# Optimization experiments

Measured on AMD Instinct MI355X. Metric: run time of the kernel, lower is better.

The kernel has to match this reference:

```python
import jax, jax.numpy as jnp
import numpy as np

DIM = 512
HEADS = 8
DIM_HEAD = 64
INNER = HEADS * DIM_HEAD  # 512
EPS = 1e-5


def _per_head_layernorm(t, gamma, beta):
    # t: [b, h, n, k]; gamma/beta: [h, k] (distinct LayerNorm per head)
    mu = jnp.mean(t, axis=-1, keepdims=True)
    var = jnp.mean(jnp.square(t - mu), axis=-1, keepdims=True)
    t_hat = (t - mu) * jax.lax.rsqrt(var + EPS)
    return t_hat * gamma[None, :, None, :] + beta[None, :, None, :]


def setup_inputs() -> dict:
    key = jax.random.key(0)
    ks = jax.random.split(key, 6)
    x = jax.random.normal(ks[0], (4, 8192, DIM), dtype=jnp.float32)
    # xavier_normal_ with gain=1e-4 on to_qkv weight [3*inner, dim]
    std_qkv = 1e-4 * np.sqrt(2.0 / (3 * INNER + DIM))
    W_qkv = jax.random.normal(ks[1], (3 * INNER, DIM), dtype=jnp.float32) * std_qkv
    gamma_K = jnp.ones((HEADS, DIM_HEAD), dtype=jnp.float32)
    beta_K = jnp.zeros((HEADS, DIM_HEAD), dtype=jnp.float32)
    gamma_V = jnp.ones((HEADS, DIM_HEAD), dtype=jnp.float32)
    beta_V = jnp.zeros((HEADS, DIM_HEAD), dtype=jnp.float32)
    std_out = np.sqrt(1.0 / INNER)
    W_out = jax.random.uniform(ks[2], (DIM, INNER), dtype=jnp.float32, minval=-std_out, maxval=std_out)
    b_out = jax.random.uniform(ks[3], (DIM,), dtype=jnp.float32, minval=-std_out, maxval=std_out)
    return {"x": x, "W_qkv": W_qkv, "gamma_K": gamma_K, "beta_K": beta_K,
            "gamma_V": gamma_V, "beta_V": beta_V, "W_out": W_out, "b_out": b_out}


def reference(x, W_qkv, gamma_K, beta_K, gamma_V, beta_V, W_out, b_out):
    b, n, _ = x.shape
    qkv = jnp.einsum('bnd,ed->bne', x, W_qkv)  # [b, n, 3*inner]
    q, k, v = jnp.split(qkv, 3, axis=-1)

    def to_heads(t):  # [b, n, h*k] -> [b, h, n, k]
        return t.reshape(b, n, HEADS, DIM_HEAD).transpose(0, 2, 1, 3)

    q, k, v = to_heads(q), to_heads(k), to_heads(v)
    k = _per_head_layernorm(k, gamma_K, beta_K)
    v = _per_head_layernorm(v, gamma_V, beta_V)

    # Galerkin linear attention: (K^T V)/n then Q @ (.)  -> O(n * d^2)
    p_attn = jnp.einsum('bhnk,bhnv->bhkv', k, v) / n  # [b, h, k, k]
    out = jnp.einsum('bhnk,bhkv->bhnv', q, p_attn)    # [b, h, n, k]
    out = out.transpose(0, 2, 1, 3).reshape(b, n, INNER)
    return jnp.einsum('bne,de->bnd', out, W_out) + b_out
```

## Files before the change

kernel.cpp:

```cpp
#include <hip/hip_runtime.h>


typedef __attribute__((ext_vector_type(8))) short bf16x8;
typedef __attribute__((ext_vector_type(4))) float f32x4;
typedef __attribute__((ext_vector_type(4))) unsigned short u16x4;

__device__ __forceinline__ unsigned short f2bf(float f) {
  unsigned int u = __builtin_bit_cast(unsigned int, f);
  u += 0x7FFFu + ((u >> 16) & 1u);
  return (unsigned short)(u >> 16);
}

__device__ __forceinline__ f32x4 mfma16(bf16x8 a, bf16x8 b, f32x4 c) {
  return __builtin_amdgcn_mfma_f32_16x16x32_bf16(a, b, c, 0, 0, 0);
}

__device__ __forceinline__ void gload16(const void* g, void* l) {
  __builtin_amdgcn_global_load_lds(
      (const __attribute__((address_space(1))) void*)g,
      (__attribute__((address_space(3))) void*)l, 16, 0, 0);
}

__global__ void k_cvt_bf16(const float* __restrict__ src,
                           unsigned short* __restrict__ dst, int n4) {
  int i = blockIdx.x * blockDim.x + threadIdx.x;
  if (i < n4) {
    float4 v = ((const float4*)src)[i];
    u16x4 o;
    o[0] = f2bf(v.x); o[1] = f2bf(v.y); o[2] = f2bf(v.z); o[3] = f2bf(v.w);
    ((u16x4*)dst)[i] = o;
  }
}

__device__ __forceinline__ void stage_tile(const unsigned short* pa,
                                           const unsigned short* pb,
                                           unsigned short* As, unsigned short* Bs,
                                           int w) {
#pragma unroll
  for (int j = 0; j < 4; ++j) {
    gload16(pa + j * 8 * 512, As + w * 2048 + j * 512);
    gload16(pb + j * 8 * 512, Bs + w * 2048 + j * 512);
  }
}

__device__ __forceinline__ void compute_tile(const unsigned short* As,
                                             const unsigned short* Bs,
                                             int wr, int wc, int g, int c16,
                                             f32x4 acc[4][4]) {
#pragma unroll
  for (int ks = 0; ks < 2; ++ks) {
    const int kcol = (ks * 32 + g * 8) ^ ((c16 & 7) << 3);
    bf16x8 af[4], bfv[4];
#pragma unroll
    for (int mi = 0; mi < 4; ++mi)
      af[mi] = *(const bf16x8*)&As[(wr * 64 + mi * 16 + c16) * 64 + kcol];
#pragma unroll
    for (int ni = 0; ni < 4; ++ni)
      bfv[ni] = *(const bf16x8*)&Bs[(wc * 64 + ni * 16 + c16) * 64 + kcol];
#pragma unroll
    for (int mi = 0; mi < 4; ++mi)
#pragma unroll
      for (int ni = 0; ni < 4; ++ni)
        acc[mi][ni] = mfma16(af[mi], bfv[ni], acc[mi][ni]);
  }
}

__launch_bounds__(256)
__global__ void k1_kvp(const unsigned short* __restrict__ xb,
                       const unsigned short* __restrict__ wqkvb,
                       const float* __restrict__ gK, const float* __restrict__ bK,
                       const float* __restrict__ gV, const float* __restrict__ bV,
                       float* __restrict__ P) {
  __shared__ __align__(16) unsigned short As[2][8192];
  __shared__ __align__(16) unsigned short Bs[2][8192];
  const int rt = blockIdx.x, h = blockIdx.y;
  const int tid = (int)threadIdx.x;
  const int l = tid & 63, w = tid >> 6;
  const int wr = w >> 1, wc = w & 1;
  const int g = l >> 4, c16 = l & 15;
  const int row0 = rt * 128;
  const int swz = ((l & 7) ^ (l >> 3)) * 8;

  const unsigned short* gsA = xb + (row0 + w * 32 + (l >> 3)) * 512 + swz;
  const int bcol = (w < 2) ? (512 + h * 64 + w * 32) : (1024 + h * 64 + (w - 2) * 32);
  const unsigned short* gsB = wqkvb + (bcol + (l >> 3)) * 512 + swz;

  f32x4 acc[4][4] = {};
  stage_tile(gsA, gsB, As[0], Bs[0], w);
  __syncthreads();
  for (int kt = 0; kt < 7; ++kt) {
    stage_tile(gsA + (kt + 1) * 64, gsB + (kt + 1) * 64,
               As[(kt + 1) & 1], Bs[(kt + 1) & 1], w);
    compute_tile(As[kt & 1], Bs[kt & 1], wr, wc, g, c16, acc);
    __syncthreads();
  }
  compute_tile(As[1], Bs[1], wr, wc, g, c16, acc);

  const float* gamma = (wc == 0) ? gK : gV;
  const float* beta  = (wc == 0) ? bK : bV;
  float gm[4], bt[4];
#pragma unroll
  for (int ni = 0; ni < 4; ++ni) {
    gm[ni] = gamma[h * 64 + ni * 16 + c16];
    bt[ni] = beta[h * 64 + ni * 16 + c16];
  }

  unsigned short* Kl = &As[0][0];
  unsigned short* Vl = &Bs[0][0];
  unsigned short* dst = (wc == 0) ? Kl : Vl;

#pragma unroll
  for (int mi = 0; mi < 4; ++mi) {
    float mean4[4], rs4[4];
#pragma unroll
    for (int r = 0; r < 4; ++r) {
      float a0 = acc[mi][0][r], a1 = acc[mi][1][r];
      float a2 = acc[mi][2][r], a3 = acc[mi][3][r];
      float s1 = a0 + a1 + a2 + a3;
      float s2 = a0 * a0 + a1 * a1 + a2 * a2 + a3 * a3;
#pragma unroll
      for (int m = 1; m <= 8; m <<= 1) {
        s1 += __shfl_xor(s1, m, 64);
        s2 += __shfl_xor(s2, m, 64);
      }
      const float mean = s1 * (1.0f / 64.0f);
      const float var = s2 * (1.0f / 64.0f) - mean * mean;
      mean4[r] = mean;
      rs4[r] = rsqrtf(var + 1e-5f);
    }
    const int n0 = wr * 64 + mi * 16 + g * 4;
#pragma unroll
    for (int ni = 0; ni < 4; ++ni) {
      const int d = ni * 16 + c16;
      u16x4 o;
#pragma unroll
      for (int r = 0; r < 4; ++r)
        o[r] = f2bf((acc[mi][ni][r] - mean4[r]) * rs4[r] * gm[ni] + bt[ni]);
      *(u16x4*)&dst[d * 128 + (((n0 >> 3) ^ c16) << 3) + (n0 & 7)] = o;
    }
  }
  __syncthreads();

  f32x4 pacc[4] = {};
#pragma unroll
  for (int ks = 0; ks < 4; ++ks) {
    const int p8 = (ks * 4 + g);
    bf16x8 af = *(const bf16x8*)&Kl[(w * 16 + c16) * 128 + ((p8 ^ c16) << 3)];
#pragma unroll
    for (int ni = 0; ni < 4; ++ni) {
      bf16x8 bfv = *(const bf16x8*)&Vl[(ni * 16 + c16) * 128 + ((p8 ^ c16) << 3)];
      pacc[ni] = mfma16(af, bfv, pacc[ni]);
    }
  }
  const int bh = (row0 >> 13) * 8 + h;
  float* Pp = P + bh * 4096;
#pragma unroll
  for (int ni = 0; ni < 4; ++ni)
#pragma unroll
    for (int r = 0; r < 4; ++r)
      atomicAdd(&Pp[(w * 16 + g * 4 + r) * 64 + ni * 16 + c16], pacc[ni][r]);
}

__launch_bounds__(256)
__global__ void k3a_g(const float* __restrict__ Wqkv,
                      const float* __restrict__ P,
                      unsigned short* __restrict__ Gt) {
  __shared__ float Pl[64 * 64];
  const int bh = blockIdx.x, dd = blockIdx.y;
  const int b = bh >> 3, h = bh & 7;
  const int t = (int)threadIdx.x;
  for (int i = t; i < 1024; i += 256)
    ((float4*)Pl)[i] = ((const float4*)(P + bh * 4096))[i];
  __syncthreads();

  const int qg = t >> 6, dl = t & 63;
  const int d = dd * 64 + dl;
  float acc[16] = {};
  for (int dh = 0; dh < 64; ++dh) {
    const float wq = Wqkv[(h * 64 + dh) * 512 + d];
    const float* pr = &Pl[dh * 64 + qg * 16];
#pragma unroll
    for (int i = 0; i < 16; ++i) acc[i] += pr[i] * wq;
  }
  unsigned short* go = &Gt[(b * 512 + d) * 512 + h * 64 + qg * 16];
#pragma unroll
  for (int i = 0; i < 16; ++i) go[i] = f2bf(acc[i] * (1.0f / 8192.0f));
}

__launch_bounds__(256)
__global__ void k3b_m(const unsigned short* __restrict__ wob,
                      const unsigned short* __restrict__ Gt,
                      unsigned short* __restrict__ Mb) {
  __shared__ __align__(16) unsigned short As[2][8192];
  __shared__ __align__(16) unsigned short Bs[2][8192];
  const int rt = blockIdx.x, ct = blockIdx.y, b = blockIdx.z;
  const int tid = (int)threadIdx.x;
  const int l = tid & 63, w = tid >> 6;
  const int wr = w >> 1, wc = w & 1;
  const int g = l >> 4, c16 = l & 15;
  const int row0 = rt * 128, col0 = ct * 128;
  const int swz = ((l & 7) ^ (l >> 3)) * 8;

  const unsigned short* gsA = wob + (row0 + w * 32 + (l >> 3)) * 512 + swz;
  const unsigned short* gsB = Gt + b * 262144 + (col0 + w * 32 + (l >> 3)) * 512 + swz;

  f32x4 acc[4][4] = {};
  stage_tile(gsA, gsB, As[0], Bs[0], w);
  __syncthreads();
  for (int kt = 0; kt < 7; ++kt) {
    stage_tile(gsA + (kt + 1) * 64, gsB + (kt + 1) * 64,
               As[(kt + 1) & 1], Bs[(kt + 1) & 1], w);
    compute_tile(As[kt & 1], Bs[kt & 1], wr, wc, g, c16, acc);
    __syncthreads();
  }
  compute_tile(As[1], Bs[1], wr, wc, g, c16, acc);

#pragma unroll
  for (int mi = 0; mi < 4; ++mi)
#pragma unroll
    for (int ni = 0; ni < 4; ++ni) {
      const int colg = col0 + wc * 64 + ni * 16 + c16;
#pragma unroll
      for (int r = 0; r < 4; ++r) {
        const int rowg = row0 + wr * 64 + mi * 16 + g * 4 + r;
        Mb[(b * 512 + rowg) * 512 + colg] = f2bf(acc[mi][ni][r]);
      }
    }
}

__launch_bounds__(256)
__global__ void k4_final(const unsigned short* __restrict__ xb,
                         const unsigned short* __restrict__ Mb,
                         const float* __restrict__ bout,
                         float* __restrict__ y) {
  __shared__ __align__(16) unsigned short As[2][8192];
  __shared__ __align__(16) unsigned short Bs[2][8192];
  const int rt = blockIdx.x, ct = blockIdx.y;
  const int tid = (int)threadIdx.x;
  const int l = tid & 63, w = tid >> 6;
  const int wr = w >> 1, wc = w & 1;
  const int g = l >> 4, c16 = l & 15;
  const int row0 = rt * 128, col0 = ct * 128;
  const int bb = row0 >> 13;
  const int swz = ((l & 7) ^ (l >> 3)) * 8;

  const unsigned short* gsA = xb + (row0 + w * 32 + (l >> 3)) * 512 + swz;
  const unsigned short* gsB = Mb + bb * 262144 + (col0 + w * 32 + (l >> 3)) * 512 + swz;

  f32x4 acc[4][4] = {};
  stage_tile(gsA, gsB, As[0], Bs[0], w);
  __syncthreads();
  for (int kt = 0; kt < 7; ++kt) {
    stage_tile(gsA + (kt + 1) * 64, gsB + (kt + 1) * 64,
               As[(kt + 1) & 1], Bs[(kt + 1) & 1], w);
    compute_tile(As[kt & 1], Bs[kt & 1], wr, wc, g, c16, acc);
    __syncthreads();
  }
  compute_tile(As[1], Bs[1], wr, wc, g, c16, acc);

  float bo[4];
#pragma unroll
  for (int ni = 0; ni < 4; ++ni)
    bo[ni] = bout[col0 + wc * 64 + ni * 16 + c16];
#pragma unroll
  for (int mi = 0; mi < 4; ++mi)
#pragma unroll
    for (int ni = 0; ni < 4; ++ni) {
      const int colg = col0 + wc * 64 + ni * 16 + c16;
#pragma unroll
      for (int r = 0; r < 4; ++r) {
        const int rowg = row0 + wr * 64 + mi * 16 + g * 4 + r;
        y[rowg * 512 + colg] = acc[mi][ni][r] + bo[ni];
      }
    }
}

extern "C" void kernel_launch(void* const* d_in, const int* in_sizes, int n_in,
                              void* d_out, int out_size, void* d_ws, size_t ws_size,
                              hipStream_t stream) {
  (void)in_sizes; (void)n_in; (void)out_size; (void)ws_size;
  const float* x    = (const float*)d_in[0];
  const float* Wqkv = (const float*)d_in[1];
  const float* gK   = (const float*)d_in[2];
  const float* bK   = (const float*)d_in[3];
  const float* gV   = (const float*)d_in[4];
  const float* bV   = (const float*)d_in[5];
  const float* Wout = (const float*)d_in[6];
  const float* bout = (const float*)d_in[7];
  float* y = (float*)d_out;

  char* w = (char*)d_ws;
  unsigned short* xb  = (unsigned short*)(w);
  unsigned short* Wb  = (unsigned short*)(w + 33554432);
  unsigned short* Wob = (unsigned short*)(w + 35127296);
  float*          P   = (float*)         (w + 35651584);
  unsigned short* Gt  = (unsigned short*)(w + 36175872);
  unsigned short* Mb  = (unsigned short*)(w + 38273024);

  k_cvt_bf16<<<16384, 256, 0, stream>>>(x, xb, 4194304);
  k_cvt_bf16<<<768, 256, 0, stream>>>(Wqkv, Wb, 196608);
  k_cvt_bf16<<<256, 256, 0, stream>>>(Wout, Wob, 65536);
  hipMemsetAsync(P, 0, 524288, stream);

  k1_kvp<<<dim3(256, 8), 256, 0, stream>>>(xb, Wb, gK, bK, gV, bV, P);
  k3a_g<<<dim3(32, 8), 256, 0, stream>>>(Wqkv, P, Gt);
  k3b_m<<<dim3(4, 4, 4), 256, 0, stream>>>(Wob, Gt, Mb);
  k4_final<<<dim3(256, 4), 256, 0, stream>>>(xb, Mb, bout, y);
}
```

Before: 145.9 us.

## Use 256x256 tiles with 8-wave pipelined MFMA loop for K/V and output GEMMs

Replaces the 128x128, 4-wave GEMM tiles in the K/V-projection and final output kernels with 256x256 tiles run by 512 threads. A new phased main loop interleaves async global-to-LDS loads with MFMA groups, using explicit waitcnt, barriers and setprio. Block IDs are remapped across groups of 8, and k1 now processes two heads' K and V per block before the per-head KᵀV reduction. The larger tiles raise data reuse and cut redundant x reads, but they need 128KB of LDS and more registers, which limits occupancy, and the hand-placed waitcnts must match the load counts exactly.

Result: slower. 161.0 us (+10.3%).

```diff
diff --git a/kernel.cpp b/kernel.cpp
--- a/kernel.cpp
+++ b/kernel.cpp
@@ -32,85 +32,129 @@
   }
 }
 
-__device__ __forceinline__ void stage_tile(const unsigned short* pa,
-                                           const unsigned short* pb,
-                                           unsigned short* As, unsigned short* Bs,
-                                           int w) {
-#pragma unroll
-  for (int j = 0; j < 4; ++j) {
-    gload16(pa + j * 8 * 512, As + w * 2048 + j * 512);
-    gload16(pb + j * 8 * 512, Bs + w * 2048 + j * 512);
-  }
-}
-
-__device__ __forceinline__ void compute_tile(const unsigned short* As,
-                                             const unsigned short* Bs,
-                                             int wr, int wc, int g, int c16,
-                                             f32x4 acc[4][4]) {
-#pragma unroll
-  for (int ks = 0; ks < 2; ++ks) {
-    const int kcol = (ks * 32 + g * 8) ^ ((c16 & 7) << 3);
-    bf16x8 af[4], bfv[4];
-#pragma unroll
-    for (int mi = 0; mi < 4; ++mi)
-      af[mi] = *(const bf16x8*)&As[(wr * 64 + mi * 16 + c16) * 64 + kcol];
-#pragma unroll
-    for (int ni = 0; ni < 4; ++ni)
-      bfv[ni] = *(const bf16x8*)&Bs[(wc * 64 + ni * 16 + c16) * 64 + kcol];
-#pragma unroll
-    for (int mi = 0; mi < 4; ++mi)
-#pragma unroll
-      for (int ni = 0; ni < 4; ++ni)
-        acc[mi][ni] = mfma16(af[mi], bfv[ni], acc[mi][ni]);
-  }
-}
-
-__launch_bounds__(256)
+__device__ __forceinline__ void gemm256_loop(
+    const unsigned short* const pA[4], const unsigned short* const pB[4],
+    unsigned short* L, int tid, f32x4 acc[8][4])
+{
+  const int l = tid & 63, w = tid >> 6;
+  const int wr = w >> 2, wc = w & 3;
+  const int g = l >> 4, c16 = l & 15;
+  const int wslot = w * 512;
+  unsigned short* LA[2] = {L, L + 16384};
+  unsigned short* LB[2] = {L + 32768, L + 49152};
+
+#pragma unroll
+  for (int i = 0; i < 4; ++i) gload16(pB[i], LB[0] + i * 4096 + wslot);
+#pragma unroll
+  for (int i = 0; i < 4; ++i) gload16(pA[i], LA[0] + i * 4096 + wslot);
+#pragma unroll
+  for (int i = 0; i < 4; ++i) gload16(pB[i] + 64, LB[1] + i * 4096 + wslot);
+  asm volatile("s_waitcnt vmcnt(4)");
+  __builtin_amdgcn_s_barrier();
+
+  for (int kt = 0; kt < 8; ++kt) {
+    const unsigned short* Ab = LA[kt & 1];
+    const unsigned short* Bb = LB[kt & 1];
+    bf16x8 bfr[4][2];
+#pragma unroll
+    for (int ph = 0; ph < 4; ++ph) {
+      if (ph == 0) {
+#pragma unroll
+        for (int ni = 0; ni < 4; ++ni)
+#pragma unroll
+          for (int ks = 0; ks < 2; ++ks)
+            bfr[ni][ks] = *(const bf16x8*)
+                &Bb[(wc * 64 + ni * 16 + c16) * 64 +
+                    ((ks * 32 + g * 8) ^ ((c16 & 7) << 3))];
+      }
+      bf16x8 af[2][2];
+#pragma unroll
+      for (int d = 0; d < 2; ++d)
+#pragma unroll
+        for (int ks = 0; ks < 2; ++ks)
+          af[d][ks] = *(const bf16x8*)
+              &Ab[(wr * 128 + (ph * 2 + d) * 16 + c16) * 64 +
+                  ((ks * 32 + g * 8) ^ ((c16 & 7) << 3))];
+      if (ph < 2) {
+        if (kt < 7) {
+#pragma unroll
+          for (int i = 0; i < 2; ++i)
+            gload16(pA[ph * 2 + i] + (kt + 1) * 64,
+                    LA[(kt + 1) & 1] + (ph * 2 + i) * 4096 + wslot);
+        }
+      } else {
+        if (kt < 6) {
+#pragma unroll
+          for (int i = 0; i < 2; ++i)
+            gload16(pB[(ph - 2) * 2 + i] + (kt + 2) * 64,
+                    LB[kt & 1] + ((ph - 2) * 2 + i) * 4096 + wslot);
+        }
+      }
+      __builtin_amdgcn_s_barrier();
+      asm volatile("s_waitcnt lgkmcnt(0)");
+      __builtin_amdgcn_sched_barrier(0);
+      __builtin_amdgcn_s_setprio(1);
+#pragma unroll
+      for (int d = 0; d < 2; ++d)
+#pragma unroll
+        for (int ni = 0; ni < 4; ++ni)
+#pragma unroll
+          for (int ks = 0; ks < 2; ++ks)
+            acc[ph * 2 + d][ni] = mfma16(af[d][ks], bfr[ni][ks],
+                                         acc[ph * 2 + d][ni]);
+      __builtin_amdgcn_s_setprio(0);
+      if (ph == 3) {
+        if (kt < 6)       { asm volatile("s_waitcnt vmcnt(4)"); }
+        else if (kt == 6) { asm volatile("s_waitcnt vmcnt(0)"); }
+      }
+      __builtin_amdgcn_s_barrier();
+    }
+  }
+}
+
+__launch_bounds__(512, 2)
 __global__ void k1_kvp(const unsigned short* __restrict__ xb,
                        const unsigned short* __restrict__ wqkvb,
                        const float* __restrict__ gK, const float* __restrict__ bK,
                        const float* __restrict__ gV, const float* __restrict__ bV,
                        float* __restrict__ P) {
-  __shared__ __align__(16) unsigned short As[2][8192];
-  __shared__ __align__(16) unsigned short Bs[2][8192];
-  const int rt = blockIdx.x, h = blockIdx.y;
+  __shared__ __align__(16) unsigned short L[65536];
+  const int bid = (int)blockIdx.x;
+  const int wgid = (bid & 7) * 64 + (bid >> 3);
+  const int rt = wgid >> 2, ct = wgid & 3;
   const int tid = (int)threadIdx.x;
   const int l = tid & 63, w = tid >> 6;
-  const int wr = w >> 1, wc = w & 1;
+  const int wr = w >> 2, wc = w & 3;
   const int g = l >> 4, c16 = l & 15;
-  const int row0 = rt * 128;
-  const int swz = ((l & 7) ^ (l >> 3)) * 8;
-
-  const unsigned short* gsA = xb + (row0 + w * 32 + (l >> 3)) * 512 + swz;
-  const int bcol = (w < 2) ? (512 + h * 64 + w * 32) : (1024 + h * 64 + (w - 2) * 32);
-  const unsigned short* gsB = wqkvb + (bcol + (l >> 3)) * 512 + swz;
-
-  f32x4 acc[4][4] = {};
-  stage_tile(gsA, gsB, As[0], Bs[0], w);
-  __syncthreads();
-  for (int kt = 0; kt < 7; ++kt) {
-    stage_tile(gsA + (kt + 1) * 64, gsB + (kt + 1) * 64,
-               As[(kt + 1) & 1], Bs[(kt + 1) & 1], w);
-    compute_tile(As[kt & 1], Bs[kt & 1], wr, wc, g, c16, acc);
-    __syncthreads();
-  }
-  compute_tile(As[1], Bs[1], wr, wc, g, c16, acc);
-
-  const float* gamma = (wc == 0) ? gK : gV;
-  const float* beta  = (wc == 0) ? bK : bV;
+  const int row0 = rt * 256;
+  const int swzc = ((tid & 7) ^ ((tid >> 3) & 7)) * 8;
+  const int r8 = tid >> 3;
+
+  const unsigned short* pA[4];
+  const unsigned short* pB[4];
+#pragma unroll
+  for (int i = 0; i < 4; ++i) {
+    pA[i] = xb + (row0 + i * 64 + r8) * 512 + swzc;
+    const int wrow = 512 + (i & 1) * 512 + (2 * ct + (i >> 1)) * 64 + r8;
+    pB[i] = wqkvb + wrow * 512 + swzc;
+  }
+
+  f32x4 acc[8][4] = {};
+  gemm256_loop(pA, pB, L, tid, acc);
+
+  const int h = 2 * ct + (wc >> 1);
+  const bool isV = wc & 1;
+  const float* gamma = isV ? gV : gK;
+  const float* beta  = isV ? bV : bK;
   float gm[4], bt[4];
 #pragma unroll
   for (int ni = 0; ni < 4; ++ni) {
     gm[ni] = gamma[h * 64 + ni * 16 + c16];
     bt[ni] = beta[h * 64 + ni * 16 + c16];
   }
-
-  unsigned short* Kl = &As[0][0];
-  unsigned short* Vl = &Bs[0][0];
-  unsigned short* dst = (wc == 0) ? Kl : Vl;
-
-#pragma unroll
-  for (int mi = 0; mi < 4; ++mi) {
+  unsigned short* Lq = L + wc * 16384;
+#pragma unroll
+  for (int mi = 0; mi < 8; ++mi) {
     float mean4[4], rs4[4];
 #pragma unroll
     for (int r = 0; r < 4; ++r) {
@@ -128,37 +172,40 @@
       mean4[r] = mean;
       rs4[r] = rsqrtf(var + 1e-5f);
     }
-    const int n0 = wr * 64 + mi * 16 + g * 4;
+    const int n0 = wr * 128 + mi * 16 + g * 4;
 #pragma unroll
     for (int ni = 0; ni < 4; ++ni) {
-      const int d = ni * 16 + c16;
       u16x4 o;
 #pragma unroll
       for (int r = 0; r < 4; ++r)
         o[r] = f2bf((acc[mi][ni][r] - mean4[r]) * rs4[r] * gm[ni] + bt[ni]);
-      *(u16x4*)&dst[d * 128 + (((n0 >> 3) ^ c16) << 3) + (n0 & 7)] = o;
+      *(u16x4*)&Lq[(ni * 16 + c16) * 256 + (((n0 >> 3) ^ c16) << 3) + (n0 & 7)] = o;
     }
   }
   __syncthreads();
 
+  const int hh = w >> 2;
+  const int strip = w & 3;
+  const unsigned short* Kq = L + (hh * 2) * 16384;
+  const unsigned short* Vq = L + (hh * 2 + 1) * 16384;
   f32x4 pacc[4] = {};
 #pragma unroll
-  for (int ks = 0; ks < 4; ++ks) {
-    const int p8 = (ks * 4 + g);
-    bf16x8 af = *(const bf16x8*)&Kl[(w * 16 + c16) * 128 + ((p8 ^ c16) << 3)];
+  for (int ks = 0; ks < 8; ++ks) {
+    const int grp = ((ks * 4 + g) ^ c16) << 3;
+    bf16x8 af = *(const bf16x8*)&Kq[(strip * 16 + c16) * 256 + grp];
 #pragma unroll
     for (int ni = 0; ni < 4; ++ni) {
-      bf16x8 bfv = *(const bf16x8*)&Vl[(ni * 16 + c16) * 128 + ((p8 ^ c16) << 3)];
-      pacc[ni] = mfma16(af, bfv, pacc[ni]);
-    }
-  }
-  const int bh = (row0 >> 13) * 8 + h;
+      bf16x8 bv = *(const bf16x8*)&Vq[(ni * 16 + c16) * 256 + grp];
+      pacc[ni] = mfma16(af, bv, pacc[ni]);
+    }
+  }
+  const int bh = (row0 >> 13) * 8 + 2 * ct + hh;
   float* Pp = P + bh * 4096;
 #pragma unroll
   for (int ni = 0; ni < 4; ++ni)
 #pragma unroll
     for (int r = 0; r < 4; ++r)
-      atomicAdd(&Pp[(w * 16 + g * 4 + r) * 64 + ni * 16 + c16], pacc[ni][r]);
+      atomicAdd(&Pp[(strip * 16 + g * 4 + r) * 64 + ni * 16 + c16], pacc[ni][r]);
 }
 
 __launch_bounds__(256)
@@ -185,6 +232,39 @@
   unsigned short* go = &Gt[(b * 512 + d) * 512 + h * 64 + qg * 16];
 #pragma unroll
   for (int i = 0; i < 16; ++i) go[i] = f2bf(acc[i] * (1.0f / 8192.0f));
+}
+
+__device__ __forceinline__ void stage_tile128(const unsigned short* pa,
+                                              const unsigned short* pb,
+                                              unsigned short* As, unsigned short* Bs,
+                                              int w) {
+#pragma unroll
+  for (int j = 0; j < 4; ++j) {
+    gload16(pa + j * 8 * 512, As + w * 2048 + j * 512);
+    gload16(pb + j * 8 * 512, Bs + w * 2048 + j * 512);
+  }
+}
+
+__device__ __forceinline__ void compute_tile128(const unsigned short* As,
+                                                const unsigned short* Bs,
+                                                int wr, int wc, int g, int c16,
+                                                f32x4 acc[4][4]) {
+#pragma unroll
+  for (int ks = 0; ks < 2; ++ks) {
+    const int kcol = (ks * 32 + g * 8) ^ ((c16 & 7) << 3);
+    bf16x8 af[4], bfv[4];
+#pragma unroll
+    for (int mi = 0; mi < 4; ++mi)
+      af[mi] = *(const bf16x8*)&As[(wr * 64 + mi * 16 + c16) * 64 + kcol];
+#pragma unroll
+    for (int ni = 0; ni < 4; ++ni)
+      bfv[ni] = *(const bf16x8*)&Bs[(wc * 64 + ni * 16 + c16) * 64 + kcol];
+#pragma unroll
+    for (int mi = 0; mi < 4; ++mi)
+#pragma unroll
+      for (int ni = 0; ni < 4; ++ni)
+        acc[mi][ni] = mfma16(af[mi], bfv[ni], acc[mi][ni]);
+  }
 }
 
 __launch_bounds__(256)
@@ -205,15 +285,15 @@
   const unsigned short* gsB = Gt + b * 262144 + (col0 + w * 32 + (l >> 3)) * 512 + swz;
 
   f32x4 acc[4][4] = {};
-  stage_tile(gsA, gsB, As[0], Bs[0], w);
+  stage_tile128(gsA, gsB, As[0], Bs[0], w);
   __syncthreads();
   for (int kt = 0; kt < 7; ++kt) {
-    stage_tile(gsA + (kt + 1) * 64, gsB + (kt + 1) * 64,
-               As[(kt + 1) & 1], Bs[(kt + 1) & 1], w);
-    compute_tile(As[kt & 1], Bs[kt & 1], wr, wc, g, c16, acc);
+    stage_tile128(gsA + (kt + 1) * 64, gsB + (kt + 1) * 64,
+                  As[(kt + 1) & 1], Bs[(kt + 1) & 1], w);
+    compute_tile128(As[kt & 1], Bs[kt & 1], wr, wc, g, c16, acc);
     __syncthreads();
   }
-  compute_tile(As[1], Bs[1], wr, wc, g, c16, acc);
+  compute_tile128(As[1], Bs[1], wr, wc, g, c16, acc);
 
 #pragma unroll
   for (int mi = 0; mi < 4; ++mi)
@@ -228,48 +308,47 @@
     }
 }
 
-__launch_bounds__(256)
+__launch_bounds__(512, 2)
 __global__ void k4_final(const unsigned short* __restrict__ xb,
                          const unsigned short* __restrict__ Mb,
                          const float* __restrict__ bout,
                          float* __restrict__ y) {
-  __shared__ __align__(16) unsigned short As[2][8192];
-  __shared__ __align__(16) unsigned short Bs[2][8192];
-  const int rt = blockIdx.x, ct = blockIdx.y;
+  __shared__ __align__(16) unsigned short L[65536];
+  const int bid = (int)blockIdx.x;
+  const int wgid = (bid & 7) * 32 + (bid >> 3);
+  const int rt = wgid >> 1, ct = wgid & 1;
   const int tid = (int)threadIdx.x;
   const int l = tid & 63, w = tid >> 6;
-  const int wr = w >> 1, wc = w & 1;
+  const int wr = w >> 2, wc = w & 3;
   const int g = l >> 4, c16 = l & 15;
-  const int row0 = rt * 128, col0 = ct * 128;
+  const int row0 = rt * 256, col0 = ct * 256;
   const int bb = row0 >> 13;
-  const int swz = ((l & 7) ^ (l >> 3)) * 8;
-
-  const unsigned short* gsA = xb + (row0 + w * 32 + (l >> 3)) * 512 + swz;
-  const unsigned short* gsB = Mb + bb * 262144 + (col0 + w * 32 + (l >> 3)) * 512 + swz;
-
-  f32x4 acc[4][4] = {};
-  stage_tile(gsA, gsB, As[0], Bs[0], w);
-  __syncthreads();
-  for (int kt = 0; kt < 7; ++kt) {
-    stage_tile(gsA + (kt + 1) * 64, gsB + (kt + 1) * 64,
-               As[(kt + 1) & 1], Bs[(kt + 1) & 1], w);
-    compute_tile(As[kt & 1], Bs[kt & 1], wr, wc, g, c16, acc);
-    __syncthreads();
-  }
-  compute_tile(As[1], Bs[1], wr, wc, g, c16, acc);
+  const int swzc = ((tid & 7) ^ ((tid >> 3) & 7)) * 8;
+  const int r8 = tid >> 3;
+
+  const unsigned short* pA[4];
+  const unsigned short* pB[4];
+#pragma unroll
+  for (int i = 0; i < 4; ++i) {
+    pA[i] = xb + (row0 + i * 64 + r8) * 512 + swzc;
+    pB[i] = Mb + (bb * 512 + col0 + i * 64 + r8) * 512 + swzc;
+  }
+
+  f32x4 acc[8][4] = {};
+  gemm256_loop(pA, pB, L, tid, acc);
 
   float bo[4];
 #pragma unroll
   for (int ni = 0; ni < 4; ++ni)
     bo[ni] = bout[col0 + wc * 64 + ni * 16 + c16];
 #pragma unroll
-  for (int mi = 0; mi < 4; ++mi)
+  for (int mi = 0; mi < 8; ++mi)
 #pragma unroll
     for (int ni = 0; ni < 4; ++ni) {
       const int colg = col0 + wc * 64 + ni * 16 + c16;
 #pragma unroll
       for (int r = 0; r < 4; ++r) {
-        const int rowg = row0 + wr * 64 + mi * 16 + g * 4 + r;
+        const int rowg = row0 + wr * 128 + mi * 16 + g * 4 + r;
         y[rowg * 512 + colg] = acc[mi][ni][r] + bo[ni];
       }
     }
@@ -302,8 +381,8 @@
   k_cvt_bf16<<<256, 256, 0, stream>>>(Wout, Wob, 65536);
   hipMemsetAsync(P, 0, 524288, stream);
 
-  k1_kvp<<<dim3(256, 8), 256, 0, stream>>>(xb, Wb, gK, bK, gV, bV, P);
+  k1_kvp<<<512, 512, 0, stream>>>(xb, Wb, gK, bK, gV, bV, P);
   k3a_g<<<dim3(32, 8), 256, 0, stream>>>(Wqkv, P, Gt);
   k3b_m<<<dim3(4, 4, 4), 256, 0, stream>>>(Wob, Gt, Mb);
-  k4_final<<<dim3(256, 4), 256, 0, stream>>>(xb, Mb, bout, y);
-}
+  k4_final<<<256, 512, 0, stream>>>(xb, Mb, bout, y);
+}
```
